# Performance work log

Hardware: AMD Instinct MI355X
Metric: run time of the kernel (lower is better)

The kernel has to match this reference:

```python
import jax, jax.numpy as jnp
import numpy as np

N_EMBD = 1024
HEAD_SIZE = 64
B, T = 4, 4096


def setup_inputs() -> dict:
    key = jax.random.key(0)
    kx, kk, kq, kv = jax.random.split(key, 4)
    s = 1.0 / np.sqrt(N_EMBD)
    return {
        "x": jax.random.normal(kx, (B, T, N_EMBD), dtype=jnp.float32),
        "Wk": jax.random.normal(kk, (N_EMBD, HEAD_SIZE), dtype=jnp.float32) * s,
        "Wq": jax.random.normal(kq, (N_EMBD, HEAD_SIZE), dtype=jnp.float32) * s,
        "Wv": jax.random.normal(kv, (N_EMBD, HEAD_SIZE), dtype=jnp.float32) * s,
    }


def reference(x, Wk, Wq, Wv):
    Bb, Tt, C = x.shape
    k = x @ Wk  # [B,T,H]
    q = x @ Wq
    v = x @ Wv
    # scores scaled by C**-0.5 where C = n_embd (as in the original module)
    w = jnp.einsum('bth,bsh->bts', q, k) * (C ** -0.5)  # [B,T,T]
    causal = jnp.tril(jnp.ones((Tt, Tt), dtype=bool))
    w = jnp.where(causal, w, -jnp.inf)
    w = jax.nn.softmax(w, axis=-1)
    # dropout prob is 0.0 (eval) -> identity
    out = jnp.einsum('bts,bsh->bth', w, v)  # [B,T,H]
    return out
```

## Files before the change

kernel.cpp:

```cpp
#include <hip/hip_runtime.h>


#define BSZ 4
#define TSZ 4096
#define CSZ 1024
#define MSZ (BSZ * TSZ)
#define QT 128
#define NQT (TSZ / QT)
#define CPB 272
#define MAXC 16

typedef _Float16 half8 __attribute__((ext_vector_type(8)));
typedef _Float16 half4 __attribute__((ext_vector_type(4)));
typedef float f32x4 __attribute__((ext_vector_type(4)));
typedef float f32x16 __attribute__((ext_vector_type(16)));

#define MFMA(a, b, c) __builtin_amdgcn_mfma_f32_16x16x32_f16((a), (b), (c), 0, 0, 0)
#define MFMA32(a, b, c) __builtin_amdgcn_mfma_f32_32x32x16_f16((a), (b), (c), 0, 0, 0)
#define QSCALE 0.04508422002778011f

__device__ __forceinline__ int kimg(int r, int h) {
    return r * 64 + (((h >> 3) ^ (r & 7)) << 3) + (h & 7);
}
__device__ __forceinline__ int vimg(int kk, int h) {
    return h * 64 + (((kk >> 3) ^ (h & 7)) << 3) + (kk & 7);
}

__device__ __forceinline__ void glds16(const _Float16* g, _Float16* l) {
    __builtin_amdgcn_global_load_lds(
        (const __attribute__((address_space(1))) void*)g,
        (__attribute__((address_space(3))) void*)l, 16, 0, 0);
}

__global__ __launch_bounds__(192) void wconv(const float* __restrict__ Wk,
                                             const float* __restrict__ Wq,
                                             const float* __restrict__ Wv,
                                             _Float16* __restrict__ Wt) {
    int k = blockIdx.x;
    int n = threadIdx.x;
    int g = k >> 6, c = (k >> 3) & 7, j = k & 7;
    const float* W = (n < 64) ? Wk : ((n < 128) ? Wq : Wv);
    float v = W[k * 64 + (n & 63)];
    if (n >= 64 && n < 128) v *= QSCALE;
    Wt[(size_t)n * 1024 + g * 64 + ((c ^ (n & 7)) << 3) + j] = (_Float16)v;
}

__global__ __launch_bounds__(512) void qkv_proj(
    const float* __restrict__ x, const _Float16* __restrict__ Wt,
    _Float16* __restrict__ qbf, _Float16* __restrict__ kvs) {
    __shared__ _Float16 wt[2][192 * 64];
    __shared__ _Float16 xt[2][64 * 64];

    int tid = threadIdx.x;
    int wave = tid >> 6, lane = tid & 63;
    int quad = lane >> 4, l16 = lane & 15;
    int id = blockIdx.x;
    int xcd = id & 7;
    int rb = (id >> 3) * 2 + (xcd & 1);
    int row0 = (xcd >> 1) * TSZ + rb * 64;
    int mh = wave >> 2;
    int ctb = (wave & 3) * 3;

    f32x4 acc[6];
#pragma unroll
    for (int i = 0; i < 6; i++) acc[i] = (f32x4){0.f, 0.f, 0.f, 0.f};

    int sr = tid >> 3, sc = tid & 7;
    const float* xrow = x + (size_t)(row0 + sr) * CSZ + sc * 8;
    f32x4 p0 = *(const f32x4*)xrow;
    f32x4 p1 = *(const f32x4*)(xrow + 4);

#pragma unroll
    for (int i = 0; i < 3; i++) {
        int g = i * 512 + tid;
        glds16(Wt + ((size_t)(g >> 3)) * 1024 + (g & 7) * 8,
               &wt[0][(size_t)g * 8]);
    }

    int cur = 0;
    for (int kc = 0; kc < CSZ; kc += 64, cur ^= 1) {
        {
            _Float16 tmp[8] __attribute__((aligned(16)));
#pragma unroll
            for (int i = 0; i < 4; i++) {
                tmp[i] = (_Float16)p0[i];
                tmp[4 + i] = (_Float16)p1[i];
            }
            *(half8*)&xt[cur][sr * 64 + ((sc ^ (sr & 7)) << 3)] = *(half8*)tmp;
        }
        __syncthreads();

        if (kc + 64 < CSZ) {
#pragma unroll
            for (int i = 0; i < 3; i++) {
                int g = i * 512 + tid;
                glds16(Wt + ((size_t)(g >> 3)) * 1024 + (kc + 64) + (g & 7) * 8,
                       &wt[cur ^ 1][(size_t)g * 8]);
            }
            p0 = *(const f32x4*)(xrow + kc + 64);
            p1 = *(const f32x4*)(xrow + kc + 68);
        }

#pragma unroll
        for (int ss = 0; ss < 2; ss++) {
            half8 a0 = *(half8*)&xt[cur][(mh * 32 + l16) * 64 +
                                         (((ss * 4 + quad) ^ (l16 & 7)) << 3)];
            half8 a1 = *(half8*)&xt[cur][(mh * 32 + 16 + l16) * 64 +
                                         (((ss * 4 + quad) ^ (l16 & 7)) << 3)];
#pragma unroll
            for (int j = 0; j < 3; j++) {
                int ct = ctb + j;
                half8 bb = *(half8*)&wt[cur][(ct * 16 + l16) * 64 +
                                             (((ss * 4 + quad) ^ (l16 & 7))
                                              << 3)];
                acc[j * 2 + 0] = MFMA(a0, bb, acc[j * 2 + 0]);
                acc[j * 2 + 1] = MFMA(a1, bb, acc[j * 2 + 1]);
            }
        }
    }

#pragma unroll
    for (int j = 0; j < 3; j++) {
        int ct = ctb + j;
        int kind = ct >> 2;
        int col = (ct & 3) * 16 + l16;
#pragma unroll
        for (int m = 0; m < 2; m++) {
#pragma unroll
            for (int r = 0; r < 4; r++) {
                int row = row0 + mh * 32 + m * 16 + quad * 4 + r;
                _Float16 val = (_Float16)acc[j * 2 + m][r];
                if (kind == 0) {
                    kvs[((size_t)(row >> 6)) * 8192 + kimg(row & 63, col)] = val;
                } else if (kind == 1) {
                    qbf[(size_t)row * 64 + col] = val;
                } else {
                    kvs[((size_t)(row >> 6)) * 8192 + 4096 +
                        vimg(row & 63, col)] = val;
                }
            }
        }
    }
}

__global__ __launch_bounds__(256, 4) void attn_partial(
    const _Float16* __restrict__ qbf, const _Float16* __restrict__ kvs,
    _Float16* __restrict__ opart, float* __restrict__ ml) {
    __shared__ _Float16 kt[2][4096];
    __shared__ _Float16 vt[2][4096];
    __shared__ float ls[4][32];

    int tid = threadIdx.x;
    int wave = tid >> 6, lane = tid & 63;
    int l32 = lane & 31, hi = lane >> 5;

    int id = blockIdx.x;
    int xcd = id & 7;
    int b = xcd >> 1;
    int id2 = (id >> 3) * 2 + (xcd & 1);
    int qt = 0;
    while (qt < NQT - 1 && (((qt + 2) * (qt + 2)) >> 2) <= id2) qt++;
    int chunk = id2 - (((qt + 1) * (qt + 1)) >> 2);
    int nt = 2 * (qt + 1);
    int lo = chunk * 4;
    int hic = min(lo + 4, nt);
    int part = (b * NQT + qt) * MAXC + chunk;

    const _Float16* qb = qbf + (size_t)b * TSZ * 64;
    const _Float16* kvb = kvs + (size_t)b * 64 * 8192;

    int qrow = qt * QT + wave * 32 + l32;
    half8 aq[4];
#pragma unroll
    for (int ss = 0; ss < 4; ss++)
        aq[ss] = *(const half8*)&qb[(size_t)qrow * 64 + ss * 16 + hi * 8];

    f32x16 o[2];
#pragma unroll
    for (int i = 0; i < 16; i++) { o[0][i] = 0.f; o[1][i] = 0.f; }
    float l_acc = 0.f;

    int soff = wave * 512 + lane * 8;

    {
        const _Float16* p0 = kvb + (size_t)lo * 8192 + soff;
        glds16(p0, &kt[0][soff]);
        glds16(p0 + 2048, &kt[0][2048 + soff]);
        glds16(p0 + 4096, &vt[0][soff]);
        glds16(p0 + 6144, &vt[0][2048 + soff]);
    }

    int cur = 0;
    for (int kti = lo; kti < hic; kti++, cur ^= 1) {
        __syncthreads();
        if (kti + 1 < hic) {
            const _Float16* p0 = kvb + (size_t)(kti + 1) * 8192 + soff;
            glds16(p0, &kt[cur ^ 1][soff]);
            glds16(p0 + 2048, &kt[cur ^ 1][2048 + soff]);
            glds16(p0 + 4096, &vt[cur ^ 1][soff]);
            glds16(p0 + 6144, &vt[cur ^ 1][2048 + soff]);
        }

        bool diag = (kti >= 2 * qt);
        int qrel = qrow - kti * 64;
        int wmax = qt * QT + wave * 32 + 31 - kti * 64;

#pragma unroll
        for (int ctk = 0; ctk < 2; ctk++) {
            if (diag && ctk * 32 > wmax) continue;

            f32x16 s;
#pragma unroll
            for (int i = 0; i < 16; i++) s[i] = 0.f;
            __builtin_amdgcn_s_setprio(1);
#pragma unroll
            for (int ss = 0; ss < 4; ss++) {
                half8 ak = *(half8*)&kt[cur][kimg(ctk * 32 + l32,
                                                  ss * 16 + hi * 8)];
                s = MFMA32(ak, aq[ss], s);
            }
            __builtin_amdgcn_s_setprio(0);

            float e[16];
#pragma unroll
            for (int r = 0; r < 16; r++) {
                float ev = exp2f(s[r]);
                if (diag) {
                    int key = ctk * 32 + (r & 3) + 8 * (r >> 2) + 4 * hi;
                    if (key > qrel) ev = 0.f;
                }
                e[r] = ev;
                l_acc += ev;
            }

            unsigned pk[8];
#pragma unroll
            for (int p = 0; p < 8; p++) {
                auto h2 = __builtin_amdgcn_cvt_pkrtz(e[2 * p], e[2 * p + 1]);
                union { decltype(h2) h; unsigned u; } cv;
                cv.h = h2;
                pk[p] = cv.u;
            }
            asm("v_permlane32_swap_b32 %0, %1" : "+v"(pk[0]), "+v"(pk[2]));
            asm("v_permlane32_swap_b32 %0, %1" : "+v"(pk[1]), "+v"(pk[3]));
            asm("v_permlane32_swap_b32 %0, %1" : "+v"(pk[4]), "+v"(pk[6]));
            asm("v_permlane32_swap_b32 %0, %1" : "+v"(pk[5]), "+v"(pk[7]));
            union { unsigned u[4]; half8 h; } A0, A1;
            A0.u[0] = pk[0]; A0.u[1] = pk[1]; A0.u[2] = pk[2]; A0.u[3] = pk[3];
            A1.u[0] = pk[4]; A1.u[1] = pk[5]; A1.u[2] = pk[6]; A1.u[3] = pk[7];

            __builtin_amdgcn_s_setprio(1);
#pragma unroll
            for (int cth = 0; cth < 2; cth++) {
                int h = cth * 32 + l32;
                half8 v0 = *(half8*)&vt[cur][vimg((2 * ctk + 0) * 16 + hi * 8, h)];
                half8 v1 = *(half8*)&vt[cur][vimg((2 * ctk + 1) * 16 + hi * 8, h)];
                o[cth] = MFMA32(A0.h, v0, o[cth]);
                o[cth] = MFMA32(A1.h, v1, o[cth]);
            }
            __builtin_amdgcn_s_setprio(0);
        }
    }

    l_acc += __shfl_xor(l_acc, 32);
    float inv = l_acc > 0.f ? 1.f / l_acc : 0.f;
    if (!hi) ls[wave][l32] = inv;

    _Float16* op = opart + (size_t)part * (QT * 64);
#pragma unroll
    for (int r = 0; r < 16; r++) {
        int rl = (r & 3) + 8 * (r >> 2) + 4 * hi;
        float invr = ls[wave][rl];
        int lrow = wave * 32 + rl;
        op[lrow * 64 + l32] = (_Float16)(o[0][r] * invr);
        op[lrow * 64 + 32 + l32] = (_Float16)(o[1][r] * invr);
    }
    if (!hi) ml[part * QT + wave * 32 + l32] = l_acc;
}

__global__ __launch_bounds__(256) void combine(
    const _Float16* __restrict__ opart, const float* __restrict__ ml,
    float* __restrict__ out) {
    int tid = threadIdx.x;
    int id = blockIdx.x;
    int xcd = id & 7;
    int b = xcd >> 1;
    int rb = (id >> 3) * 2 + (xcd & 1);
    int row = b * TSZ + rb * 32 + (tid >> 3);
    int seg = (tid & 7) * 8;
    int qt = (row >> 7) & (NQT - 1);
    int prow = row & (QT - 1);
    int pbase = (b * NQT + qt) * MAXC;
    int nc = (qt + 2) >> 1;

    float acc[8];
#pragma unroll
    for (int i = 0; i < 8; i++) acc[i] = 0.f;
    float lsum = 0.f;
    for (int s = 0; s < nc; s++) {
        float l = ml[(pbase + s) * QT + prow];
        lsum += l;
        half8 h = *(const half8*)&opart[(size_t)(pbase + s) * (QT * 64) +
                                        prow * 64 + seg];
#pragma unroll
        for (int i = 0; i < 8; i++) acc[i] += l * (float)h[i];
    }
    float inv = 1.f / lsum;
    float* ob = out + (size_t)row * 64 + seg;
#pragma unroll
    for (int i = 0; i < 8; i++) ob[i] = acc[i] * inv;
}

extern "C" void kernel_launch(void* const* d_in, const int* in_sizes, int n_in,
                              void* d_out, int out_size, void* d_ws,
                              size_t ws_size, hipStream_t stream) {
    (void)in_sizes; (void)n_in; (void)out_size; (void)ws_size;
    const float* x = (const float*)d_in[0];
    const float* Wk = (const float*)d_in[1];
    const float* Wq = (const float*)d_in[2];
    const float* Wv = (const float*)d_in[3];

    _Float16* Wt = (_Float16*)d_ws;
    _Float16* qbf = Wt + 192 * 1024;
    _Float16* kvs = qbf + (size_t)MSZ * 64;
    _Float16* opart = kvs + (size_t)MSZ * 128;
    float* ml = (float*)(opart + (size_t)BSZ * NQT * MAXC * QT * 64);

    wconv<<<1024, 192, 0, stream>>>(Wk, Wq, Wv, Wt);
    qkv_proj<<<MSZ / 64, 512, 0, stream>>>(x, Wt, qbf, kvs);
    attn_partial<<<BSZ * CPB, 256, 0, stream>>>(qbf, kvs, opart, ml);
    combine<<<MSZ / 32, 256, 0, stream>>>(opart, ml, (float*)d_out);
}
```

Baseline: 144.1 us.

## Fuse split-KV combine into attention via last-block atomic counter

Removes the separate combine kernel launch. Each attention block increments a per-query-tile atomic counter, and the last block to finish merges the partial outputs into the final result. Query tiles with a single chunk write fp32 output directly and skip the partial write. It also swaps exp2f for the raw hardware exp2 builtin, and resets the counters inside wconv. The cost is a serialized tail on the last block of each tile, plus added synchronization and fence overhead.

```diff
diff --git a/kernel.cpp b/kernel.cpp
--- a/kernel.cpp
+++ b/kernel.cpp
@@ -35,9 +35,11 @@
 __global__ __launch_bounds__(192) void wconv(const float* __restrict__ Wk,
                                              const float* __restrict__ Wq,
                                              const float* __restrict__ Wv,
-                                             _Float16* __restrict__ Wt) {
+                                             _Float16* __restrict__ Wt,
+                                             int* __restrict__ cnt) {
     int k = blockIdx.x;
     int n = threadIdx.x;
+    if (k == 0 && n < BSZ * NQT) cnt[n] = 0;
     int g = k >> 6, c = (k >> 3) & 7, j = k & 7;
     const float* W = (n < 64) ? Wk : ((n < 128) ? Wq : Wv);
     float v = W[k * 64 + (n & 63)];
@@ -145,10 +147,12 @@
 
 __global__ __launch_bounds__(256, 4) void attn_partial(
     const _Float16* __restrict__ qbf, const _Float16* __restrict__ kvs,
-    _Float16* __restrict__ opart, float* __restrict__ ml) {
+    _Float16* __restrict__ opart, float* __restrict__ ml,
+    float* __restrict__ out, int* __restrict__ cnt) {
     __shared__ _Float16 kt[2][4096];
     __shared__ _Float16 vt[2][4096];
     __shared__ float ls[4][32];
+    __shared__ int lastf;
 
     int tid = threadIdx.x;
     int wave = tid >> 6, lane = tid & 63;
@@ -164,6 +168,7 @@
     int nt = 2 * (qt + 1);
     int lo = chunk * 4;
     int hic = min(lo + 4, nt);
+    int nc = (qt + 2) >> 1;
     int part = (b * NQT + qt) * MAXC + chunk;
 
     const _Float16* qb = qbf + (size_t)b * TSZ * 64;
@@ -224,7 +229,7 @@
             float e[16];
 #pragma unroll
             for (int r = 0; r < 16; r++) {
-                float ev = exp2f(s[r]);
+                float ev = __builtin_amdgcn_exp2f(s[r]);
                 if (diag) {
                     int key = ctk * 32 + (r & 3) + 8 * (r >> 2) + 4 * hi;
                     if (key > qrel) ev = 0.f;
@@ -266,6 +271,19 @@
     float inv = l_acc > 0.f ? 1.f / l_acc : 0.f;
     if (!hi) ls[wave][l32] = inv;
 
+    if (nc == 1) {
+        float* ob = out + ((size_t)(b * TSZ + qt * QT)) * 64;
+#pragma unroll
+        for (int r = 0; r < 16; r++) {
+            int rl = (r & 3) + 8 * (r >> 2) + 4 * hi;
+            float invr = ls[wave][rl];
+            int lrow = wave * 32 + rl;
+            ob[lrow * 64 + l32] = o[0][r] * invr;
+            ob[lrow * 64 + 32 + l32] = o[1][r] * invr;
+        }
+        return;
+    }
+
     _Float16* op = opart + (size_t)part * (QT * 64);
 #pragma unroll
     for (int r = 0; r < 16; r++) {
@@ -276,39 +294,42 @@
         op[lrow * 64 + 32 + l32] = (_Float16)(o[1][r] * invr);
     }
     if (!hi) ml[part * QT + wave * 32 + l32] = l_acc;
-}
-
-__global__ __launch_bounds__(256) void combine(
-    const _Float16* __restrict__ opart, const float* __restrict__ ml,
-    float* __restrict__ out) {
-    int tid = threadIdx.x;
-    int id = blockIdx.x;
-    int xcd = id & 7;
-    int b = xcd >> 1;
-    int rb = (id >> 3) * 2 + (xcd & 1);
-    int row = b * TSZ + rb * 32 + (tid >> 3);
-    int seg = (tid & 7) * 8;
-    int qt = (row >> 7) & (NQT - 1);
-    int prow = row & (QT - 1);
-    int pbase = (b * NQT + qt) * MAXC;
-    int nc = (qt + 2) >> 1;
-
-    float acc[8];
-#pragma unroll
-    for (int i = 0; i < 8; i++) acc[i] = 0.f;
-    float lsum = 0.f;
-    for (int s = 0; s < nc; s++) {
-        float l = ml[(pbase + s) * QT + prow];
-        lsum += l;
-        half8 h = *(const half8*)&opart[(size_t)(pbase + s) * (QT * 64) +
-                                        prow * 64 + seg];
-#pragma unroll
-        for (int i = 0; i < 8; i++) acc[i] += l * (float)h[i];
-    }
-    float inv = 1.f / lsum;
-    float* ob = out + (size_t)row * 64 + seg;
-#pragma unroll
-    for (int i = 0; i < 8; i++) ob[i] = acc[i] * inv;
+
+    __syncthreads();
+    if (tid == 0) {
+        __threadfence();
+        int old = __hip_atomic_fetch_add(cnt + (b * NQT + qt), 1,
+                                         __ATOMIC_ACQ_REL,
+                                         __HIP_MEMORY_SCOPE_AGENT);
+        lastf = (old == nc - 1);
+    }
+    __syncthreads();
+    if (!lastf) return;
+    __threadfence();
+
+    const _Float16* opq = opart + (size_t)(b * NQT + qt) * MAXC * (QT * 64);
+    const float* mlq = ml + (size_t)(b * NQT + qt) * MAXC * QT;
+    float* ob = out + ((size_t)(b * TSZ + qt * QT)) * 64;
+#pragma unroll
+    for (int pass = 0; pass < 4; pass++) {
+        int prow = pass * 32 + (tid >> 3);
+        int seg = (tid & 7) * 8;
+        float acc[8];
+#pragma unroll
+        for (int i = 0; i < 8; i++) acc[i] = 0.f;
+        float lsum = 0.f;
+        for (int s2 = 0; s2 < nc; s2++) {
+            float l = mlq[s2 * QT + prow];
+            lsum += l;
+            half8 h = *(const half8*)&opq[(size_t)s2 * (QT * 64) +
+                                          prow * 64 + seg];
+#pragma unroll
+            for (int i = 0; i < 8; i++) acc[i] += l * (float)h[i];
+        }
+        float invf = 1.f / lsum;
+#pragma unroll
+        for (int i = 0; i < 8; i++) ob[prow * 64 + seg + i] = acc[i] * invf;
+    }
 }
 
 extern "C" void kernel_launch(void* const* d_in, const int* in_sizes, int n_in,
@@ -325,9 +346,10 @@
     _Float16* kvs = qbf + (size_t)MSZ * 64;
     _Float16* opart = kvs + (size_t)MSZ * 128;
     float* ml = (float*)(opart + (size_t)BSZ * NQT * MAXC * QT * 64);
-
-    wconv<<<1024, 192, 0, stream>>>(Wk, Wq, Wv, Wt);
+    int* cnt = (int*)(ml + (size_t)BSZ * NQT * MAXC * QT);
+
+    wconv<<<1024, 192, 0, stream>>>(Wk, Wq, Wv, Wt, cnt);
     qkv_proj<<<MSZ / 64, 512, 0, stream>>>(x, Wt, qbf, kvs);
-    attn_partial<<<BSZ * CPB, 256, 0, stream>>>(qbf, kvs, opart, ml);
-    combine<<<MSZ / 32, 256, 0, stream>>>(opart, ml, (float*)d_out);
-}
+    attn_partial<<<BSZ * CPB, 256, 0, stream>>>(qbf, kvs, opart, ml,
+                                                (float*)d_out, cnt);
+}
```

New measurement: 234.3 us. 62.6% more time.
